# Optimization experiments

Measured on AMD Instinct MI355X. Metric: run time of the kernel, lower is better.

## Reference

```python
import jax, jax.numpy as jnp
from jax import lax
import numpy as np

G = 32        # voxel grid resolution per axis (pres=vres=1 -> voxel = floor(coord))
N = 100000    # number of points
C = 96        # hidden_dim == input_dim


def _voxelize(feats, coords):
    """initial_voxelize: average point features per voxel. Returns (grid (G^3,C), occ (G^3,) bool, flat idx)."""
    vox = jnp.clip(jnp.floor(coords).astype(jnp.int32), 0, G - 1)
    flat = (vox[:, 0] * G + vox[:, 1]) * G + vox[:, 2]
    sums = jax.ops.segment_sum(feats, flat, num_segments=G ** 3)
    cnt = jax.ops.segment_sum(jnp.ones((feats.shape[0],), feats.dtype), flat, num_segments=G ** 3)
    grid = sums / jnp.maximum(cnt, 1.0)[:, None]
    return grid, cnt > 0


def _sconv(feats, coords, conv_w, lin_w, lin_b):
    """SConv3d: voxelize -> submanifold 3x3x3 conv (outputs only at occupied voxels)
    -> trilinear devoxelize (missing voxels contribute 0) -> + Linear(feats)."""
    Cin = feats.shape[1]
    Cout = conv_w.shape[0]
    grid, occ = _voxelize(feats, coords)
    g = grid.reshape(G, G, G, Cin).transpose(3, 0, 1, 2)[None]          # (1,Cin,G,G,G)
    out = lax.conv_general_dilated(g, conv_w, (1, 1, 1), 'SAME',
                                   dimension_numbers=('NCDHW', 'OIDHW', 'NCDHW'))
    out = out * occ.reshape(1, 1, G, G, G)                               # submanifold: keep input coords only
    outv = out[0].transpose(1, 2, 3, 0).reshape(G ** 3, Cout)            # (G^3,Cout)
    base = jnp.floor(coords)
    f = coords - base                                                    # trilinear fractions (N,3)
    basei = base.astype(jnp.int32)
    devox = jnp.zeros((feats.shape[0], Cout), feats.dtype)
    for dx in (0, 1):
        for dy in (0, 1):
            for dz in (0, 1):
                c = basei + jnp.array([dx, dy, dz], jnp.int32)
                valid = jnp.all((c >= 0) & (c < G), axis=1)
                cc = jnp.clip(c, 0, G - 1)
                flc = (cc[:, 0] * G + cc[:, 1]) * G + cc[:, 2]
                w = ((f[:, 0] if dx else 1.0 - f[:, 0]) *
                     (f[:, 1] if dy else 1.0 - f[:, 1]) *
                     (f[:, 2] if dz else 1.0 - f[:, 2]))
                w = w * (valid & occ[flc]).astype(w.dtype)
                devox = devox + outv[flc] * w[:, None]
    return devox + feats @ lin_w.T + lin_b


def setup_inputs() -> dict:
    key = jax.random.key(0)
    ks = jax.random.split(key, 20)
    def conv(k, o, i):
        return jax.random.normal(k, (o, i, 3, 3, 3), jnp.float32) / np.sqrt(i * 27)
    def lin(k, o, i):
        k1, k2 = jax.random.split(k)
        return (jax.random.normal(k1, (o, i), jnp.float32) / np.sqrt(i),
                jax.random.normal(k2, (o,), jnp.float32) * 0.01)
    wq_lw, wq_lb = lin(ks[3], C, C)
    wh_lw, wh_lb = lin(ks[4], C, C)
    att_lw, att_lb = lin(ks[5], C, 2 * C)
    v_lw, v_lb = lin(ks[6], 1, C)
    upd_lw, upd_lb = lin(ks[7], C, 2 * C)
    return {
        'hidden': jax.random.normal(ks[0], (N, C), jnp.float32),
        'query': jax.random.normal(ks[1], (N, C), jnp.float32),
        'coords': jax.random.uniform(ks[2], (N, 3), jnp.float32) * G,
        'wq_conv': conv(ks[8], C, C), 'wq_lw': wq_lw, 'wq_lb': wq_lb,
        'wh_conv': conv(ks[9], C, C), 'wh_lw': wh_lw, 'wh_lb': wh_lb,
        'att_conv': conv(ks[10], C, 2 * C), 'att_lw': att_lw, 'att_lb': att_lb,
        'v_conv': conv(ks[11], 1, C), 'v_lw': v_lw, 'v_lb': v_lb,
        'upd_conv': conv(ks[12], C, 2 * C), 'upd_lw': upd_lw, 'upd_lb': upd_lb,
    }


def reference(hidden, query, coords,
              wq_conv, wq_lw, wq_lb,
              wh_conv, wh_lw, wh_lb,
              att_conv, att_lw, att_lb,
              v_conv, v_lw, v_lb,
              upd_conv, upd_lw, upd_lb):
    q = _sconv(query, coords, wq_conv, wq_lw, wq_lb)           # (N,C)
    h = _sconv(hidden, coords, wh_conv, wh_lw, wh_lb)          # (N,C)
    hx = jnp.concatenate([h, q], axis=1)                        # (N,2C)
    energy = jnp.tanh(_sconv(hx, coords, att_conv, att_lw, att_lb))
    attn = _sconv(energy, coords, v_conv, v_lw, v_lb)           # (N,1)
    context = attn * h                                          # attention-gated hidden
    qcat = jnp.concatenate([q, context], axis=1)                # (N,2C)
    return jnp.tanh(_sconv(qcat, coords, upd_conv, upd_lw, upd_lb))
```

## Files before the change

kernel.cpp:

```cpp
#include <hip/hip_runtime.h>
#include <math.h>


#define GD 32
#define NV (GD*GD*GD)
#define CH 96

typedef _Float16 half8 __attribute__((ext_vector_type(8)));
typedef _Float16 half4 __attribute__((ext_vector_type(4)));
typedef float f32x4 __attribute__((ext_vector_type(4)));


__global__ void k_prep(const float* __restrict__ coords, int* __restrict__ flat,
                       unsigned* __restrict__ cnt, int n) {
  int i = blockIdx.x * 256 + threadIdx.x;
  if (i >= n) return;
  float x = coords[3*i], y = coords[3*i+1], z = coords[3*i+2];
  int ix = (int)floorf(x); ix = ix < 0 ? 0 : (ix > 31 ? 31 : ix);
  int iy = (int)floorf(y); iy = iy < 0 ? 0 : (iy > 31 ? 31 : iy);
  int iz = (int)floorf(z); iz = iz < 0 ? 0 : (iz > 31 ? 31 : iz);
  int f = (ix << 10) + (iy << 5) + iz;
  flat[i] = f;
  atomicAdd(&cnt[f], 1u);
}

__global__ __launch_bounds__(1024) void k_scan(
    const unsigned* __restrict__ cnt, unsigned* __restrict__ base,
    unsigned* __restrict__ cur, float* __restrict__ inv) {
  __shared__ unsigned part[1024];
  int tid = threadIdx.x;
  int b0 = tid * 32;
  unsigned s = 0;
  for (int i = 0; i < 32; ++i) s += cnt[b0 + i];
  part[tid] = s;
  __syncthreads();
  for (int off = 1; off < 1024; off <<= 1) {
    unsigned t = (tid >= off) ? part[tid - off] : 0u;
    __syncthreads();
    if (tid >= off) part[tid] += t;
    __syncthreads();
  }
  unsigned run = part[tid] - s;
  for (int i = 0; i < 32; ++i) {
    int v = b0 + i;
    unsigned c = cnt[v];
    base[v] = run; cur[v] = run;
    inv[v] = c ? 1.0f / (float)c : 0.0f;
    run += c;
  }
}

__global__ void k_fill(const int* __restrict__ flat, unsigned* __restrict__ cur,
                       int* __restrict__ order, int n) {
  int p = blockIdx.x * 256 + threadIdx.x;
  if (p >= n) return;
  unsigned pos = atomicAdd(&cur[flat[p]], 1u);
  order[pos] = p;
}

template<int SCALED, int PAIR, int SRCF16, int SORTED>
__global__ void k_voxavg(const void* __restrict__ src, const float* __restrict__ scale,
                         const unsigned* __restrict__ base, const unsigned* __restrict__ cnt,
                         const float* __restrict__ inv, const int* __restrict__ order,
                         void* __restrict__ dst,
                         const void* __restrict__ src2, void* __restrict__ dst2) {
  constexpr int NC = SRCF16 ? 12 : 24;
  int e = blockIdx.x * 256 + threadIdx.x;
  const void* sp = src; void* d = dst;
  if (PAIR && e >= NV * NC) { e -= NV * NC; sp = src2; d = dst2; }
  int v = e / NC, cc = e - v * NC;
  unsigned b = base[v], c = cnt[v];
  if (SRCF16) {
    f32x4 slo = {0.f, 0.f, 0.f, 0.f}, shi = {0.f, 0.f, 0.f, 0.f};
    for (unsigned i = 0; i < c; ++i) {
      int p = SORTED ? (int)(b + i) : order[b + i];
      half8 hx = __builtin_nontemporal_load(reinterpret_cast<const half8*>(sp) + p * 12 + cc);
      f32x4 lo = {(float)hx[0], (float)hx[1], (float)hx[2], (float)hx[3]};
      f32x4 hi = {(float)hx[4], (float)hx[5], (float)hx[6], (float)hx[7]};
      if (SCALED) { float sc = scale[p]; lo *= sc; hi *= sc; }
      slo += lo; shi += hi;
    }
    float iv = inv[v];
    slo *= iv; shi *= iv;
    half8 o = {(_Float16)slo.x, (_Float16)slo.y, (_Float16)slo.z, (_Float16)slo.w,
               (_Float16)shi.x, (_Float16)shi.y, (_Float16)shi.z, (_Float16)shi.w};
    reinterpret_cast<half8*>(d)[e] = o;
  } else {
    f32x4 s = {0.f, 0.f, 0.f, 0.f};
    for (unsigned i = 0; i < c; ++i) {
      int p = SORTED ? (int)(b + i) : order[b + i];
      f32x4 x = __builtin_nontemporal_load(reinterpret_cast<const f32x4*>(sp) + p * 24 + cc);
      if (SCALED) x *= scale[p];
      s += x;
    }
    s *= inv[v];
    union { _Float16 h; unsigned short u; } h0, h1, h2, h3;
    h0.h = (_Float16)s.x; h1.h = (_Float16)s.y; h2.h = (_Float16)s.z; h3.h = (_Float16)s.w;
    ushort4 o; o.x = h0.u; o.y = h1.u; o.z = h2.u; o.w = h3.u;
    reinterpret_cast<ushort4*>(d)[e] = o;
  }
}


__device__ __forceinline__ void wpack_one(int e, const float* __restrict__ w,
                                          _Float16* __restrict__ wp, int nch) {
  int j = e & 7; int l = (e >> 3) & 63; int r = e >> 9;
  int cot = r % 6; r /= 6; int chk = r % nch; int tap = r / nch;
  int Ci = nch * 32;
  int ci = chk * 32 + (l >> 4) * 8 + j;
  int co = cot * 16 + (l & 15);
  wp[e] = (_Float16)w[(co * Ci + ci) * 27 + tap];
}

__device__ __forceinline__ void linpack_one(int e, const float* __restrict__ w,
                                            _Float16* __restrict__ wl, int kb) {
  int j = e & 7; int l = (e >> 3) & 63; int r = e >> 9;
  int nt = r % 6; int kt = r / 6;
  int Ci = kb * 32;
  int ci = kt * 32 + (l >> 4) * 8 + j;
  int co = nt * 16 + (l & 15);
  wl[e] = (_Float16)w[co * Ci + ci];
}

#define WP3 (27*3*6*512)
#define WP6 (27*6*6*512)
#define WL3 (3*6*512)
#define WL6 (6*6*512)
#define WV2 (27*512)
#define PACK_TOTAL (2*WP3 + 2*WP6 + 2*WL3 + 2*WL6 + WV2)

__global__ void k_packall(
    const float* __restrict__ wq, const float* __restrict__ wh,
    const float* __restrict__ wa, const float* __restrict__ wu,
    const float* __restrict__ lq, const float* __restrict__ lh,
    const float* __restrict__ la, const float* __restrict__ lu,
    const float* __restrict__ wvc,
    _Float16* __restrict__ wpq, _Float16* __restrict__ wph,
    _Float16* __restrict__ wpa, _Float16* __restrict__ wpu,
    _Float16* __restrict__ wlq, _Float16* __restrict__ wlh,
    _Float16* __restrict__ wla, _Float16* __restrict__ wlu,
    _Float16* __restrict__ wt2) {
  int e = blockIdx.x * 256 + threadIdx.x;
  if (e < WP3) { wpack_one(e, wq, wpq, 3); return; } e -= WP3;
  if (e < WP3) { wpack_one(e, wh, wph, 3); return; } e -= WP3;
  if (e < WP6) { wpack_one(e, wa, wpa, 6); return; } e -= WP6;
  if (e < WP6) { wpack_one(e, wu, wpu, 6); return; } e -= WP6;
  if (e < WL3) { linpack_one(e, lq, wlq, 3); return; } e -= WL3;
  if (e < WL3) { linpack_one(e, lh, wlh, 3); return; } e -= WL3;
  if (e < WL6) { linpack_one(e, la, wla, 6); return; } e -= WL6;
  if (e < WL6) { linpack_one(e, lu, wlu, 6); return; } e -= WL6;
  if (e < WV2) {
    int j = e & 7; int l = (e >> 3) & 63; int r = e >> 9;
    int col9 = r % 9, chunk = r / 9;
    int n = l & 15, kq = l >> 4;
    int ci = chunk * 32 + kq * 8 + j;
    wt2[e] = (n < 3) ? (_Float16)wvc[ci * 27 + col9 * 3 + n] : (_Float16)0.f;
  }
}

template<int NCH, int PAIR>
__global__ __launch_bounds__(384, 4) void k_conv_mfma(
    const _Float16* __restrict__ gA, const _Float16* __restrict__ gB,
    const half8* __restrict__ wp, _Float16* __restrict__ out,
    const _Float16* __restrict__ gA2, const half8* __restrict__ wp2,
    _Float16* __restrict__ out2) {
  __shared__ unsigned short ls[12 * 34 * 40];
  int bid = blockIdx.x;
  const _Float16* ga = gA; const _Float16* gb = gB;
  const half8* w = wp; _Float16* o = out;
  if (PAIR && bid >= 512) { bid -= 512; ga = gA2; gb = gA2; w = wp2; o = out2; }
  int bx = bid >> 4, y0 = (bid & 15) * 2;
  int tid = threadIdx.x;
  int lane = tid & 63, wv = tid >> 6;
  int msel = wv & 1, npair = wv >> 1;
  int lrow = lane & 15, quad = lane >> 4;

  f32x4 acc[2][2];
#pragma unroll
  for (int i = 0; i < 2; ++i)
#pragma unroll
    for (int j = 0; j < 2; ++j) acc[i][j] = (f32x4){0.f, 0.f, 0.f, 0.f};

  for (int chunk = 0; chunk < NCH; ++chunk) {
    const _Float16* g = (NCH == 6 && chunk >= 3) ? gb : ga;
    int cbase = ((NCH == 6 && chunk >= 3) ? chunk - 3 : chunk) * 32;
    __syncthreads();
    for (int e = tid; e < 12 * 34 * 4; e += 384) {
      int ciu = e & 3; int zc = e >> 2;
      int zz = zc % 34; int sc = zc / 34;
      int dx = sc >> 2, dyy = sc & 3;
      int x = bx + dx - 1, y = y0 + dyy - 1, zv = zz - 1;
      uint4 val = {0u, 0u, 0u, 0u};
      if ((unsigned)x < 32u && (unsigned)y < 32u && (unsigned)zv < 32u)
        val = *reinterpret_cast<const uint4*>(
            g + (size_t)((x << 10) + (y << 5) + zv) * CH + cbase + ciu * 8);
      *reinterpret_cast<uint4*>(&ls[(sc * 34 + zz) * 40 + ciu * 8]) = val;
    }
    __syncthreads();
#pragma unroll
    for (int dx9 = 0; dx9 < 3; ++dx9)
#pragma unroll
      for (int dy9 = 0; dy9 < 3; ++dy9) {
        int sc = dx9 * 4 + msel + dy9;
        const unsigned short* lbase = &ls[(sc * 34) * 40 + quad * 8];
        int tap0 = (dx9 * 3 + dy9) * 3;
#pragma unroll
        for (int dz = 0; dz < 3; ++dz) {
          half8 a0 = *reinterpret_cast<const half8*>(&lbase[(lrow + dz) * 40]);
          half8 a1 = *reinterpret_cast<const half8*>(&lbase[(16 + lrow + dz) * 40]);
          const half8* wb = w + ((size_t)((tap0 + dz) * NCH + chunk) * 6 + npair * 2) * 64 + lane;
          half8 b0 = wb[0];
          half8 b1 = wb[64];
          acc[0][0] = __builtin_amdgcn_mfma_f32_16x16x32_f16(a0, b0, acc[0][0], 0, 0, 0);
          acc[1][0] = __builtin_amdgcn_mfma_f32_16x16x32_f16(a1, b0, acc[1][0], 0, 0, 0);
          acc[0][1] = __builtin_amdgcn_mfma_f32_16x16x32_f16(a0, b1, acc[0][1], 0, 0, 0);
          acc[1][1] = __builtin_amdgcn_mfma_f32_16x16x32_f16(a1, b1, acc[1][1], 0, 0, 0);
        }
      }
  }
  int y = y0 + msel;
  int vb = (bx << 10) + (y << 5);
#pragma unroll
  for (int mt = 0; mt < 2; ++mt)
#pragma unroll
    for (int nb = 0; nb < 2; ++nb)
#pragma unroll
      for (int r = 0; r < 4; ++r) {
        int z = mt * 16 + quad * 4 + r;
        o[(size_t)(vb + z) * CH + (npair * 2 + nb) * 16 + lrow] = (_Float16)acc[mt][nb][r];
      }
}

__global__ __launch_bounds__(128) void k_conv3d_v2(
    const _Float16* __restrict__ g, const _Float16* __restrict__ wt2,
    float* __restrict__ out) {
  __shared__ unsigned short ls[12 * 48 * 32];
  __shared__ float dl[2][48][4];
  int bid = blockIdx.x;
  int bx = bid >> 4, y0 = (bid & 15) * 2;
  int tid = threadIdx.x;
  int lane = tid & 63, wv = tid >> 6;
  int lrow = lane & 15, quad = lane >> 4;

  f32x4 acc[3];
#pragma unroll
  for (int i = 0; i < 3; ++i) acc[i] = (f32x4){0.f, 0.f, 0.f, 0.f};

  for (int chunk = 0; chunk < 3; ++chunk) {
    __syncthreads();
#pragma unroll 3
    for (int it = 0; it < 18; ++it) {
      int e = it * 128 + tid;
      int c8 = e & 3;
      int t = e >> 2;
      int col = t / 48;
      int zz = t - col * 48;
      int dx = col >> 2, dyy = col & 3;
      int x = bx + dx - 1, y = y0 + dyy - 1, zv = zz - 1;
      uint4 val = {0u, 0u, 0u, 0u};
      if ((unsigned)x < 32u && (unsigned)y < 32u && (unsigned)zv < 32u)
        val = *reinterpret_cast<const uint4*>(
            g + (size_t)((x << 10) + (y << 5) + zv) * CH + chunk * 32 + c8 * 8);
      *reinterpret_cast<uint4*>(&ls[(t << 5) + ((c8 ^ (zz & 3)) << 3)]) = val;
    }
    __syncthreads();
#pragma unroll
    for (int dx9 = 0; dx9 < 3; ++dx9)
#pragma unroll
      for (int dy9 = 0; dy9 < 3; ++dy9) {
        int col9 = dx9 * 3 + dy9;
        int sc = dx9 * 4 + wv + dy9;
        half8 b = *reinterpret_cast<const half8*>(
            wt2 + (size_t)((chunk * 9 + col9) << 9) + (lane << 3));
#pragma unroll
        for (int mt = 0; mt < 3; ++mt) {
          int zz = mt * 16 + lrow;
          half8 a = *reinterpret_cast<const half8*>(
              &ls[((sc * 48 + zz) << 5) + ((quad ^ (zz & 3)) << 3)]);
          acc[mt] = __builtin_amdgcn_mfma_f32_16x16x32_f16(a, b, acc[mt], 0, 0, 0);
        }
      }
  }
  if (lrow < 3) {
#pragma unroll
    for (int mt = 0; mt < 3; ++mt)
#pragma unroll
      for (int r = 0; r < 4; ++r)
        dl[wv][mt * 16 + quad * 4 + r][lrow] = acc[mt][r];
  }
  __syncthreads();
  if (tid < 64) {
    int z = tid & 31, yb = tid >> 5;
    float v = dl[yb][z][0] + dl[yb][z + 1][1] + dl[yb][z + 2][2];
    out[(bx << 10) + ((y0 + yb) << 5) + z] = v;
  }
}


__device__ __forceinline__ void corner_one(
    const float* __restrict__ coords, const unsigned* __restrict__ cnt,
    int p, int k, int& flc, float& w) {
  float cx = coords[3*p], cy = coords[3*p+1], cz = coords[3*p+2];
  float bx = floorf(cx), by = floorf(cy), bz = floorf(cz);
  float fx = cx - bx, fy = cy - by, fz = cz - bz;
  int dx = (k >> 2) & 1, dy = (k >> 1) & 1, dzz = k & 1;
  int ix = (int)bx + dx, iy = (int)by + dy, iz = (int)bz + dzz;
  bool valid = ((unsigned)ix < 32u) && ((unsigned)iy < 32u) && ((unsigned)iz < 32u);
  int xc = min(max(ix, 0), 31), yc = min(max(iy, 0), 31), zc = min(max(iz, 0), 31);
  flc = (xc << 10) + (yc << 5) + zc;
  float wx = dx ? fx : 1.f - fx;
  float wy = dy ? fy : 1.f - fy;
  float wz = dzz ? fz : 1.f - fz;
  w = (valid && cnt[flc] > 0u) ? wx * wy * wz : 0.f;
}

template<int KB, int MODE, int PAIR>
__global__ __launch_bounds__(256) void k_point(
    const _Float16* __restrict__ outv, const void* __restrict__ X1, const void* __restrict__ X2,
    const float* __restrict__ scale, const half8* __restrict__ wl,
    const float* __restrict__ lb, const float* __restrict__ vlw,
    const float* __restrict__ coords, const unsigned* __restrict__ cnt,
    const int* __restrict__ order,
    void* __restrict__ dst, float* __restrict__ attn_out, int n,
    const _Float16* __restrict__ outv2, const void* __restrict__ X1b,
    const half8* __restrict__ wl2, const float* __restrict__ lb2,
    void* __restrict__ dst2) {
  __shared__ char us[64 * 100 * 4];
  __shared__ int lflc[512];
  __shared__ float lcw[512];
  __shared__ int lord[64];
  constexpr int APITCH = KB * 32 + 8;
  constexpr int XF16 = (KB == 6);
  constexpr int OUTF16 = (MODE != 2);
  int tid = threadIdx.x;
  int bid = blockIdx.x;
  const _Float16* ov = outv; const void* x1 = X1;
  const half8* w = wl; const float* b = lb; void* d = dst;
  if (PAIR) {
    int npt = (n + 63) >> 6;
    if (bid >= npt) { bid -= npt; ov = outv2; x1 = X1b; w = wl2; b = lb2; d = dst2; }
  }
  int p0 = bid * 64;

  if (tid < 64) lord[tid] = (p0 + tid < n) ? order[p0 + tid] : 0;
  __syncthreads();

  for (int e = tid; e < 512; e += 256) {
    int j = e >> 3, k = e & 7;
    int f = 0; float wgt = 0.f;
    if (p0 + j < n) corner_one(coords, cnt, lord[j], k, f, wgt);
    lflc[e] = f; lcw[e] = wgt;
  }

  unsigned short* lsa = reinterpret_cast<unsigned short*>(us);
  if (XF16) {
    for (int e = tid; e < 64 * KB * 4; e += 256) {
      int j = e / (KB * 4);
      int q8 = e - j * (KB * 4);
      int idx = p0 + j;
      half8 hx = {(_Float16)0.f, (_Float16)0.f, (_Float16)0.f, (_Float16)0.f,
                  (_Float16)0.f, (_Float16)0.f, (_Float16)0.f, (_Float16)0.f};
      if (idx < n) {
        if (q8 < 12) {
          hx = __builtin_nontemporal_load(reinterpret_cast<const half8*>(x1) + idx * 12 + q8);
        } else {
          hx = __builtin_nontemporal_load(reinterpret_cast<const half8*>(X2) + idx * 12 + (q8 - 12));
          if (MODE == 2) {
            float sc = scale[idx];
#pragma unroll
            for (int u = 0; u < 8; ++u) hx[u] = (_Float16)((float)hx[u] * sc);
          }
        }
      }
      *reinterpret_cast<half8*>(&lsa[j * APITCH + q8 * 8]) = hx;
    }
  } else {
    for (int e = tid; e < 64 * KB * 8; e += 256) {
      int j = e / (KB * 8);
      int q4 = e - j * (KB * 8);
      int idx = p0 + j;
      f32x4 v = {0.f, 0.f, 0.f, 0.f};
      if (idx < n)
        v = __builtin_nontemporal_load(
            reinterpret_cast<const f32x4*>(x1) + (size_t)lord[j] * 24 + q4);
      union { _Float16 h; unsigned short u; } h0, h1, h2, h3;
      h0.h = (_Float16)v.x; h1.h = (_Float16)v.y; h2.h = (_Float16)v.z; h3.h = (_Float16)v.w;
      ushort4 o; o.x = h0.u; o.y = h1.u; o.z = h2.u; o.w = h3.u;
      *reinterpret_cast<ushort4*>(&lsa[j * APITCH + q4 * 4]) = o;
    }
  }
  __syncthreads();

  int lane = tid & 63, wv = tid >> 6;
  int lrow = lane & 15, quad = lane >> 4;
  f32x4 acc[6];
#pragma unroll
  for (int i = 0; i < 6; ++i) acc[i] = (f32x4){0.f, 0.f, 0.f, 0.f};
#pragma unroll
  for (int kt = 0; kt < KB; ++kt) {
    half8 a = *reinterpret_cast<const half8*>(&lsa[(wv * 16 + lrow) * APITCH + kt * 32 + quad * 8]);
    const half8* wb = w + (size_t)(kt * 6) * 64 + lane;
#pragma unroll
    for (int nt = 0; nt < 6; ++nt)
      acc[nt] = __builtin_amdgcn_mfma_f32_16x16x32_f16(a, wb[(size_t)nt * 64], acc[nt], 0, 0, 0);
  }
  __syncthreads();
  float* lacc = reinterpret_cast<float*>(us);
#pragma unroll
  for (int nt = 0; nt < 6; ++nt)
#pragma unroll
    for (int r = 0; r < 4; ++r)
      lacc[(wv * 16 + quad * 4 + r) * 100 + nt * 16 + lrow] = acc[nt][r];
  __syncthreads();

  int pt = tid >> 2, sub = tid & 3;
  int idx = p0 + pt;
  bool valid = idx < n;
  f32x4 a[6];
  const float* lrow_p = &lacc[pt * 100 + sub * 24];
#pragma unroll
  for (int i = 0; i < 6; ++i) a[i] = *reinterpret_cast<const f32x4*>(lrow_p + i * 4);
  const f32x4* lb4 = reinterpret_cast<const f32x4*>(b + sub * 24);
#pragma unroll
  for (int i = 0; i < 6; ++i) a[i] += lb4[i];
#pragma unroll
  for (int k = 0; k < 8; ++k) {
    float wgt = lcw[pt * 8 + k];
    if (wgt != 0.f) {
      const half8* op = reinterpret_cast<const half8*>(ov + (size_t)lflc[pt * 8 + k] * CH + sub * 24);
      half8 o0 = op[0], o1 = op[1], o2 = op[2];
      f32x4 t;
      t = (f32x4){(float)o0[0], (float)o0[1], (float)o0[2], (float)o0[3]}; a[0] += wgt * t;
      t = (f32x4){(float)o0[4], (float)o0[5], (float)o0[6], (float)o0[7]}; a[1] += wgt * t;
      t = (f32x4){(float)o1[0], (float)o1[1], (float)o1[2], (float)o1[3]}; a[2] += wgt * t;
      t = (f32x4){(float)o1[4], (float)o1[5], (float)o1[6], (float)o1[7]}; a[3] += wgt * t;
      t = (f32x4){(float)o2[0], (float)o2[1], (float)o2[2], (float)o2[3]}; a[4] += wgt * t;
      t = (f32x4){(float)o2[4], (float)o2[5], (float)o2[6], (float)o2[7]}; a[5] += wgt * t;
    }
  }
  if (MODE >= 1) {
#pragma unroll
    for (int i = 0; i < 6; ++i) {
      a[i].x = tanhf(a[i].x); a[i].y = tanhf(a[i].y);
      a[i].z = tanhf(a[i].z); a[i].w = tanhf(a[i].w);
    }
  }
  if (valid) {
    if (OUTF16) {
      _Float16* dh = reinterpret_cast<_Float16*>(d) + (size_t)idx * CH + sub * 24;
      uint4* du = reinterpret_cast<uint4*>(dh);
#pragma unroll
      for (int i = 0; i < 3; ++i) {
        union { _Float16 h[8]; uint4 q; } t;
        t.h[0] = (_Float16)a[2*i].x;   t.h[1] = (_Float16)a[2*i].y;
        t.h[2] = (_Float16)a[2*i].z;   t.h[3] = (_Float16)a[2*i].w;
        t.h[4] = (_Float16)a[2*i+1].x; t.h[5] = (_Float16)a[2*i+1].y;
        t.h[6] = (_Float16)a[2*i+1].z; t.h[7] = (_Float16)a[2*i+1].w;
        du[i] = t.q;
      }
    } else {
      f32x4* d4 = reinterpret_cast<f32x4*>(d) + (size_t)lord[pt] * 24 + sub * 6;
#pragma unroll
      for (int i = 0; i < 6; ++i) d4[i] = a[i];
    }
  }
  if (MODE == 1) {
    const f32x4* vw4 = reinterpret_cast<const f32x4*>(vlw + sub * 24);
    float partial = 0.f;
#pragma unroll
    for (int i = 0; i < 6; ++i) {
      f32x4 vw = vw4[i];
      partial += a[i].x * vw.x + a[i].y * vw.y + a[i].z * vw.z + a[i].w * vw.w;
    }
    partial += __shfl_xor(partial, 1);
    partial += __shfl_xor(partial, 2);
    if (sub == 0 && valid) attn_out[idx] = partial;
  }
}

__global__ void k_attn_final(const float* __restrict__ outvV, const float* __restrict__ vlb,
                             const float* __restrict__ coords, const unsigned* __restrict__ cnt,
                             const int* __restrict__ order,
                             float* __restrict__ attn, int n) {
  int idx = blockIdx.x * 256 + threadIdx.x;
  if (idx >= n) return;
  int p = order[idx];
  float a = attn[idx] + vlb[0];
#pragma unroll
  for (int k = 0; k < 8; ++k) {
    int f; float w;
    corner_one(coords, cnt, p, k, f, w);
    a += w * outvV[f];
  }
  attn[idx] = a;
}


extern "C" void kernel_launch(void* const* d_in, const int* in_sizes, int n_in,
                              void* d_out, int out_size, void* d_ws, size_t ws_size,
                              hipStream_t stream) {
  const float* hidden   = (const float*)d_in[0];
  const float* query    = (const float*)d_in[1];
  const float* coords   = (const float*)d_in[2];
  const float* wq_conv  = (const float*)d_in[3];
  const float* wq_lw    = (const float*)d_in[4];
  const float* wq_lb    = (const float*)d_in[5];
  const float* wh_conv  = (const float*)d_in[6];
  const float* wh_lw    = (const float*)d_in[7];
  const float* wh_lb    = (const float*)d_in[8];
  const float* att_conv = (const float*)d_in[9];
  const float* att_lw   = (const float*)d_in[10];
  const float* att_lb   = (const float*)d_in[11];
  const float* v_conv   = (const float*)d_in[12];
  const float* v_lw     = (const float*)d_in[13];
  const float* v_lb     = (const float*)d_in[14];
  const float* upd_conv = (const float*)d_in[15];
  const float* upd_lw   = (const float*)d_in[16];
  const float* upd_lb   = (const float*)d_in[17];
  float* out = (float*)d_out;
  const int n = in_sizes[0] / CH;

  char* wsp = (char*)d_ws;
  auto alloc = [&](size_t bytes) {
    char* r = wsp;
    wsp += (bytes + 255) & ~(size_t)255;
    return r;
  };
  int*      flat  = (int*)     alloc((size_t)n * 4);
  int*      order = (int*)     alloc((size_t)n * 4);
  unsigned* cnt   = (unsigned*)alloc((size_t)NV * 4);
  unsigned* base  = (unsigned*)alloc((size_t)NV * 4);
  unsigned* cur   = (unsigned*)alloc((size_t)NV * 4);
  float*    inv   = (float*)   alloc((size_t)NV * 4);
  float*    attn  = (float*)   alloc((size_t)n * 4);
  _Float16* wt2   = (_Float16*)alloc((size_t)WV2 * 2);
  _Float16* wpq = (_Float16*)alloc((size_t)WP3 * 2);
  _Float16* wph = (_Float16*)alloc((size_t)WP3 * 2);
  _Float16* wpa = (_Float16*)alloc((size_t)WP6 * 2);
  _Float16* wpu = (_Float16*)alloc((size_t)WP6 * 2);
  _Float16* wlq = (_Float16*)alloc((size_t)WL3 * 2);
  _Float16* wlh = (_Float16*)alloc((size_t)WL3 * 2);
  _Float16* wla = (_Float16*)alloc((size_t)WL6 * 2);
  _Float16* wlu = (_Float16*)alloc((size_t)WL6 * 2);
  _Float16* Hq  = (_Float16*)alloc((size_t)NV * CH * 2);
  _Float16* Hh  = (_Float16*)alloc((size_t)NV * CH * 2);
  _Float16* H1  = (_Float16*)alloc((size_t)NV * CH * 2);
  _Float16* H2  = (_Float16*)alloc((size_t)NV * CH * 2);
  _Float16* O1  = (_Float16*)alloc((size_t)NV * CH * 2);
  _Float16* O2  = (_Float16*)alloc((size_t)NV * CH * 2);
  float* Ov   = (float*)alloc((size_t)NV * 4);
  _Float16* qv   = (_Float16*)alloc((size_t)n * CH * 2);
  _Float16* hv   = (_Float16*)alloc((size_t)n * CH * 2);
  _Float16* ebuf = (_Float16*)alloc((size_t)n * CH * 2);

  const int nb  = (n + 255) / 256;
  const int npt = (n + 63) / 64;
  const int nva   = NV * 24 / 256;
  const int nva16 = NV * 12 / 256;

  hipMemsetAsync(cnt, 0, (size_t)NV * 4, stream);
  k_prep<<<nb, 256, 0, stream>>>(coords, flat, cnt, n);
  k_scan<<<1, 1024, 0, stream>>>(cnt, base, cur, inv);
  k_fill<<<nb, 256, 0, stream>>>(flat, cur, order, n);
  k_packall<<<(PACK_TOTAL + 255) / 256, 256, 0, stream>>>(
      wq_conv, wh_conv, att_conv, upd_conv, wq_lw, wh_lw, att_lw, upd_lw, v_conv,
      wpq, wph, wpa, wpu, wlq, wlh, wla, wlu, wt2);

  k_voxavg<0,1,0,0><<<2*nva, 256, 0, stream>>>(query, nullptr, base, cnt, inv, order,
                                               Hq, hidden, Hh);
  k_conv_mfma<3,1><<<1024, 384, 0, stream>>>(Hq, Hq, (const half8*)wpq, O1,
                                             Hh, (const half8*)wph, O2);
  k_point<3,0,1><<<2*npt, 256, 0, stream>>>(O1, query, nullptr, nullptr, (const half8*)wlq,
                                            wq_lb, nullptr, coords, cnt, order, qv, nullptr, n,
                                            O2, hidden, (const half8*)wlh, wh_lb, hv);

  k_voxavg<0,1,1,1><<<2*nva16, 256, 0, stream>>>(hv, nullptr, base, cnt, inv, order,
                                                 H1, qv, H2);
  k_conv_mfma<6,0><<<512, 384, 0, stream>>>(H1, H2, (const half8*)wpa, O1,
                                            nullptr, nullptr, nullptr);
  k_point<6,1,0><<<npt, 256, 0, stream>>>(O1, hv, qv, nullptr, (const half8*)wla,
                                          att_lb, v_lw, coords, cnt, order, ebuf, attn, n,
                                          nullptr, nullptr, nullptr, nullptr, nullptr);

  k_voxavg<0,0,1,1><<<nva16, 256, 0, stream>>>(ebuf, nullptr, base, cnt, inv, order,
                                               Hq, nullptr, nullptr);
  k_conv3d_v2<<<512, 128, 0, stream>>>(Hq, wt2, Ov);
  k_attn_final<<<nb, 256, 0, stream>>>(Ov, v_lb, coords, cnt, order, attn, n);

  k_voxavg<1,0,1,1><<<nva16, 256, 0, stream>>>(hv, attn, base, cnt, inv, order,
                                               H1, nullptr, nullptr);
  k_conv_mfma<6,0><<<512, 384, 0, stream>>>(H2, H1, (const half8*)wpu, O1,
                                            nullptr, nullptr, nullptr);
  k_point<6,2,0><<<npt, 256, 0, stream>>>(O1, qv, hv, attn, (const half8*)wlu,
                                          upd_lb, nullptr, coords, cnt, order, out, nullptr, n,
                                          nullptr, nullptr, nullptr, nullptr, nullptr);
}
```

Baseline: 580.6 us.

## Double-buffer LDS staging in MFMA conv to overlap global loads with compute

The conv kernel now keeps two LDS buffers. It prefetches the next channel chunk's halo tile into registers while the MFMA loop runs on the current buffer, then writes those registers into the other buffer. Per-thread staging addresses and bounds checks are computed once up front instead of on every chunk. The goal is to hide global-load latency and drop one barrier per chunk. The cost is doubled LDS use (about 65KB per block), which may lower the occupancy the launch bounds allow, plus extra registers for five prefetched uint4 values.

```diff
diff --git a/kernel.cpp b/kernel.cpp
--- a/kernel.cpp
+++ b/kernel.cpp
@@ -158,13 +158,14 @@
   }
 }
 
+#define CSTG (12*34*4)
 template<int NCH, int PAIR>
 __global__ __launch_bounds__(384, 4) void k_conv_mfma(
     const _Float16* __restrict__ gA, const _Float16* __restrict__ gB,
     const half8* __restrict__ wp, _Float16* __restrict__ out,
     const _Float16* __restrict__ gA2, const half8* __restrict__ wp2,
     _Float16* __restrict__ out2) {
-  __shared__ unsigned short ls[12 * 34 * 40];
+  __shared__ unsigned short ls[2][12 * 34 * 40];
   int bid = blockIdx.x;
   const _Float16* ga = gA; const _Float16* gb = gB;
   const half8* w = wp; _Float16* o = out;
@@ -175,34 +176,72 @@
   int msel = wv & 1, npair = wv >> 1;
   int lrow = lane & 15, quad = lane >> 4;
 
+  int s_off[5];
+  size_t s_g[5];
+  bool s_act[5];
+#pragma unroll
+  for (int it = 0; it < 5; ++it) {
+    int e = it * 384 + tid;
+    s_act[it] = (e < CSTG);
+    int ee = s_act[it] ? e : 0;
+    int ciu = ee & 3; int zc = ee >> 2;
+    int zz = zc % 34; int sc = zc / 34;
+    int dx = sc >> 2, dyy = sc & 3;
+    int x = bx + dx - 1, y = y0 + dyy - 1, zv = zz - 1;
+    bool inb = ((unsigned)x < 32u) && ((unsigned)y < 32u) && ((unsigned)zv < 32u);
+    s_g[it] = inb ? (size_t)((x << 10) + (y << 5) + zv) * CH + ciu * 8 : (size_t)0;
+    if (!inb) s_act[it] = s_act[it];
+    s_off[it] = (sc * 34 + zz) * 40 + ciu * 8;
+    if (!inb) s_g[it] = ~(size_t)0;
+  }
+
+  auto g_of = [&](int chunk) -> const _Float16* {
+    return (NCH == 6 && chunk >= 3) ? gb : ga;
+  };
+  auto cb_of = [&](int chunk) -> int {
+    return ((NCH == 6 && chunk >= 3) ? chunk - 3 : chunk) * 32;
+  };
+
   f32x4 acc[2][2];
 #pragma unroll
   for (int i = 0; i < 2; ++i)
 #pragma unroll
     for (int j = 0; j < 2; ++j) acc[i][j] = (f32x4){0.f, 0.f, 0.f, 0.f};
 
+  {
+    const _Float16* g = g_of(0); int cbase = cb_of(0);
+#pragma unroll
+    for (int it = 0; it < 5; ++it) {
+      if (s_act[it]) {
+        uint4 val = {0u, 0u, 0u, 0u};
+        if (s_g[it] != ~(size_t)0)
+          val = *reinterpret_cast<const uint4*>(g + s_g[it] + cbase);
+        *reinterpret_cast<uint4*>(&ls[0][s_off[it]]) = val;
+      }
+    }
+  }
+  __syncthreads();
+
   for (int chunk = 0; chunk < NCH; ++chunk) {
-    const _Float16* g = (NCH == 6 && chunk >= 3) ? gb : ga;
-    int cbase = ((NCH == 6 && chunk >= 3) ? chunk - 3 : chunk) * 32;
-    __syncthreads();
-    for (int e = tid; e < 12 * 34 * 4; e += 384) {
-      int ciu = e & 3; int zc = e >> 2;
-      int zz = zc % 34; int sc = zc / 34;
-      int dx = sc >> 2, dyy = sc & 3;
-      int x = bx + dx - 1, y = y0 + dyy - 1, zv = zz - 1;
-      uint4 val = {0u, 0u, 0u, 0u};
-      if ((unsigned)x < 32u && (unsigned)y < 32u && (unsigned)zv < 32u)
-        val = *reinterpret_cast<const uint4*>(
-            g + (size_t)((x << 10) + (y << 5) + zv) * CH + cbase + ciu * 8);
-      *reinterpret_cast<uint4*>(&ls[(sc * 34 + zz) * 40 + ciu * 8]) = val;
-    }
-    __syncthreads();
+    int cur = chunk & 1;
+    bool has_next = (chunk + 1 < NCH);
+    uint4 sreg[5];
+    if (has_next) {
+      const _Float16* g = g_of(chunk + 1); int cbase = cb_of(chunk + 1);
+#pragma unroll
+      for (int it = 0; it < 5; ++it) {
+        uint4 val = {0u, 0u, 0u, 0u};
+        if (s_act[it] && s_g[it] != ~(size_t)0)
+          val = *reinterpret_cast<const uint4*>(g + s_g[it] + cbase);
+        sreg[it] = val;
+      }
+    }
 #pragma unroll
     for (int dx9 = 0; dx9 < 3; ++dx9)
 #pragma unroll
       for (int dy9 = 0; dy9 < 3; ++dy9) {
         int sc = dx9 * 4 + msel + dy9;
-        const unsigned short* lbase = &ls[(sc * 34) * 40 + quad * 8];
+        const unsigned short* lbase = &ls[cur][(sc * 34) * 40 + quad * 8];
         int tap0 = (dx9 * 3 + dy9) * 3;
 #pragma unroll
         for (int dz = 0; dz < 3; ++dz) {
@@ -217,7 +256,15 @@
           acc[1][1] = __builtin_amdgcn_mfma_f32_16x16x32_f16(a1, b1, acc[1][1], 0, 0, 0);
         }
       }
-  }
+    if (has_next) {
+#pragma unroll
+      for (int it = 0; it < 5; ++it)
+        if (s_act[it])
+          *reinterpret_cast<uint4*>(&ls[cur ^ 1][s_off[it]]) = sreg[it];
+    }
+    __syncthreads();
+  }
+
   int y = y0 + msel;
   int vb = (bx << 10) + (y << 5);
 #pragma unroll
```

After: 645.6 us. +11.2%, slower.
